# Kernel tuning notes

Measured on AMD Instinct MI355X. Metric: run time of the kernel, lower is better.

Reference implementation:

```python
import jax, jax.numpy as jnp
import numpy as np

LORA_ALPHA = 16.0

def setup_inputs() -> dict:
    key = jax.random.key(0)
    kx, kw, ka, kb, kbias = jax.random.split(key, 5)
    B_, S, D_in, D_out, R = 2, 4096, 4096, 4096, 16
    x = jax.random.normal(kx, (B_, S, D_in), dtype=jnp.float32)
    W = jax.random.normal(kw, (D_out, D_in), dtype=jnp.float32) * 0.02
    A = jax.random.normal(ka, (R, D_in), dtype=jnp.float32) * 0.02
    Bm = jax.random.normal(kb, (D_out, R), dtype=jnp.float32) * 0.02
    bias = jax.random.normal(kbias, (D_out,), dtype=jnp.float32) * 0.02
    return {"x": x, "W": W, "A": A, "B": Bm, "bias": bias}

def reference(x, W, A, B, bias):
    # y = x @ W.T + bias + (alpha/rank) * (x @ A.T) @ B.T   (dropout p=0)
    rank = A.shape[0]
    lora_scale = LORA_ALPHA / rank
    y = jnp.einsum('bsd,nd->bsn', x, W) + bias
    h = jnp.einsum('bsd,rd->bsr', x, A)          # [B,S,r] low-rank down-proj
    y = y + lora_scale * jnp.einsum('bsr,nr->bsn', h, B)
    return y
```

## Files before the change

### kernel.cpp

```cpp
#include <hip/hip_runtime.h>
#include <hip/hip_bf16.h>

typedef short bf16x8 __attribute__((ext_vector_type(8)));
typedef float f32x4 __attribute__((ext_vector_type(4)));
typedef unsigned short ushort8v __attribute__((ext_vector_type(8)));

#define SBAR() asm volatile("s_barrier" ::: "memory")
#define LGKM0() do { asm volatile("s_waitcnt lgkmcnt(0)" ::: "memory"); \
    __builtin_amdgcn_sched_barrier(0); } while (0)

__device__ __forceinline__ unsigned short f2bf(float f) {
  unsigned u = __builtin_bit_cast(unsigned, f);
  u += 0x7fffu + ((u >> 16) & 1u);
  return (unsigned short)(u >> 16);
}

__device__ __forceinline__ void gload_lds16(const unsigned short* g, unsigned short* l) {
  __builtin_amdgcn_global_load_lds((const __attribute__((address_space(1))) void*)g,
                                   (__attribute__((address_space(3))) void*)l, 16, 0, 0);
}

__global__ __launch_bounds__(256) void prep_kernel(const float* __restrict__ x,
                                                   const float* __restrict__ W,
                                                   const float* __restrict__ A,
                                                   const float* __restrict__ Bm,
                                                   unsigned short* __restrict__ xb,
                                                   unsigned short* __restrict__ wb,
                                                   float scale, int K, int R, int n8, int t8) {
  int i = blockIdx.x * 256 + threadIdx.x;
  if (i < n8) {
    const float4* p = (const float4*)x + (size_t)i * 2;
    float4 a = p[0], b = p[1];
    ushort8v v;
    v[0] = f2bf(a.x); v[1] = f2bf(a.y); v[2] = f2bf(a.z); v[3] = f2bf(a.w);
    v[4] = f2bf(b.x); v[5] = f2bf(b.y); v[6] = f2bf(b.z); v[7] = f2bf(b.w);
    *((ushort8v*)xb + i) = v;
    return;
  }
  int idx = i - n8;
  if (idx >= t8) return;
  int perRow = K >> 3;
  int n = idx / perRow;
  int d0 = (idx - n * perRow) << 3;
  const float4* wp = (const float4*)(W + (size_t)n * K + d0);
  float4 w0 = wp[0], w1 = wp[1];
  float acc[8] = {w0.x, w0.y, w0.z, w0.w, w1.x, w1.y, w1.z, w1.w};
#pragma unroll 4
  for (int r = 0; r < R; ++r) {
    float c = Bm[(size_t)n * R + r] * scale;
    const float4* ap = (const float4*)(A + (size_t)r * K + d0);
    float4 a0 = ap[0], a1 = ap[1];
    acc[0] += c * a0.x; acc[1] += c * a0.y; acc[2] += c * a0.z; acc[3] += c * a0.w;
    acc[4] += c * a1.x; acc[5] += c * a1.y; acc[6] += c * a1.z; acc[7] += c * a1.w;
  }
  ushort8v v;
#pragma unroll
  for (int j = 0; j < 8; ++j) v[j] = f2bf(acc[j]);
  *((ushort8v*)wb + idx) = v;
}

__global__ __launch_bounds__(512, 2) void gemm256_bt_bias(const unsigned short* __restrict__ Xb,
                                                          const unsigned short* __restrict__ Wb,
                                                          const float* __restrict__ bias,
                                                          float* __restrict__ C,
                                                          int M, int N, int K) {
  __shared__ __align__(16) unsigned short lds[4][16384];
  const int t = threadIdx.x;
  const int wave = t >> 6, lane = t & 63;
  const int fr = lane & 15, kc = lane >> 4;
  const int wr = wave >> 2, wc = wave & 3;

  const int NTn = N >> 8;
  const int nwg = gridDim.x;
  int bid = blockIdx.x;
  if ((nwg & 7) == 0) bid = (bid & 7) * (nwg >> 3) + (bid >> 3);
  const int tm = bid / NTn, tn = bid % NTn;
  const int m0 = tm << 8, n0 = tn << 8;

  const int srow = t >> 2;
  const int gch  = (t & 3) ^ ((t >> 3) & 3);
  const unsigned short* gA0 = Xb + (size_t)(m0 + srow) * K + gch * 8;
  const unsigned short* gA1 = gA0 + (size_t)128 * K;
  const unsigned short* gB0 = Wb + (size_t)(n0 + srow) * K + gch * 8;
  const unsigned short* gB1 = gB0 + (size_t)128 * K;
  const int stA0 = wave * 512;
  const int stA1 = 4096 + wave * 512;
  const int stB0 = 8192 + wave * 512;
  const int stB1 = 12288 + wave * 512;

  int offA[8], offB[4];
#pragma unroll
  for (int m = 0; m < 8; ++m) {
    int row = wr * 128 + m * 16 + fr;
    offA[m] = row * 64 + (((kc ^ (row >> 1)) & 3) << 4);
  }
#pragma unroll
  for (int n = 0; n < 4; ++n) {
    int row = wc * 64 + n * 16 + fr;
    offB[n] = 16384 + row * 64 + (((kc ^ (row >> 1)) & 3) << 4);
  }

  f32x4 acc[8][4];
#pragma unroll
  for (int m = 0; m < 8; ++m)
#pragma unroll
    for (int n = 0; n < 4; ++n) acc[m][n] = (f32x4){0.f, 0.f, 0.f, 0.f};

  const int NT = K >> 5;

#define STAGE_A(tt) do {                                 \
    unsigned short* sb_ = &lds[(tt) & 3][0];             \
    const int ko_ = (tt) * 32;                           \
    gload_lds16(gA0 + ko_, sb_ + stA0);                  \
    gload_lds16(gA1 + ko_, sb_ + stA1);                  \
  } while (0)
#define STAGE_B(tt) do {                                 \
    unsigned short* sb_ = &lds[(tt) & 3][0];             \
    const int ko_ = (tt) * 32;                           \
    gload_lds16(gB0 + ko_, sb_ + stB0);                  \
    gload_lds16(gB1 + ko_, sb_ + stB1);                  \
  } while (0)

#define TILE(tt, DOSTAGE, VM) do {                                                \
    const char* p_ = (const char*)&lds[(tt) & 3][0];                              \
    bf16x8 av_[4], bv_[4];                                                        \
    _Pragma("unroll") for (int n = 0; n < 4; ++n)                                 \
      bv_[n] = *(const bf16x8*)(p_ + offB[n]);                                    \
    _Pragma("unroll") for (int m = 0; m < 4; ++m)                                 \
      av_[m] = *(const bf16x8*)(p_ + offA[m]);                                    \
    if (DOSTAGE) { STAGE_A((tt) + 3); }                                           \
    SBAR();                                                                       \
    LGKM0();                                                                      \
    __builtin_amdgcn_s_setprio(1);                                                \
    _Pragma("unroll") for (int m = 0; m < 4; ++m)                                 \
      _Pragma("unroll") for (int n = 0; n < 4; ++n)                               \
        acc[m][n] = __builtin_amdgcn_mfma_f32_16x16x32_bf16(av_[m], bv_[n], acc[m][n], 0, 0, 0); \
    __builtin_amdgcn_s_setprio(0);                                                \
    SBAR();                                                                       \
    _Pragma("unroll") for (int m = 0; m < 4; ++m)                                 \
      av_[m] = *(const bf16x8*)(p_ + offA[4 + m]);                                \
    if (DOSTAGE) { STAGE_B((tt) + 3); }                                           \
    asm volatile("s_waitcnt vmcnt(" VM ")" ::: "memory");                         \
    SBAR();                                                                       \
    LGKM0();                                                                      \
    __builtin_amdgcn_s_setprio(1);                                                \
    _Pragma("unroll") for (int m = 0; m < 4; ++m)                                 \
      _Pragma("unroll") for (int n = 0; n < 4; ++n)                               \
        acc[4 + m][n] = __builtin_amdgcn_mfma_f32_16x16x32_bf16(av_[m], bv_[n], acc[4 + m][n], 0, 0, 0); \
    __builtin_amdgcn_s_setprio(0);                                                \
    SBAR();                                                                       \
  } while (0)

  STAGE_A(0); STAGE_B(0); STAGE_A(1); STAGE_B(1); STAGE_A(2); STAGE_B(2);
  asm volatile("s_waitcnt vmcnt(8)" ::: "memory");
  SBAR();

  for (int tt = 0; tt < NT - 3; ++tt) TILE(tt, 1, "8");
  TILE(NT - 3, 0, "4");
  TILE(NT - 2, 0, "0");
  TILE(NT - 1, 0, "0");

  const int crow = (lane >> 4) * 4;
  const int ccol = lane & 15;
#pragma unroll
  for (int n = 0; n < 4; ++n) {
    int col = n0 + wc * 64 + n * 16 + ccol;
    float bv = bias[col];
#pragma unroll
    for (int m = 0; m < 8; ++m) {
      int row = m0 + wr * 128 + m * 16 + crow;
      float* cp = C + (size_t)row * N + col;
#pragma unroll
      for (int r = 0; r < 4; ++r) cp[(size_t)r * N] = acc[m][n][r] + bv;
    }
  }
#undef STAGE_A
#undef STAGE_B
#undef TILE
}

__global__ __launch_bounds__(256) void gemm_bt_bias(const unsigned short* __restrict__ Xb,
                                                    const unsigned short* __restrict__ Wb,
                                                    const float* __restrict__ bias,
                                                    float* __restrict__ C,
                                                    int M, int N, int K) {
  __shared__ unsigned short sA[128 * 32];
  __shared__ unsigned short sB[128 * 32];
  const int t = threadIdx.x;
  const int wave = t >> 6, lane = t & 63;
  const int NT = N >> 7;
  const int nwg = gridDim.x;
  int bid = blockIdx.x;
  if ((nwg & 7) == 0) bid = (bid & 7) * (nwg >> 3) + (bid >> 3);
  const int tm = bid / NT, tn = bid % NT;
  const int m0 = tm << 7, n0 = tn << 7;
  const int wr = wave >> 1, wc = wave & 1;

  f32x4 acc[4][4];
#pragma unroll
  for (int m = 0; m < 4; ++m)
#pragma unroll
    for (int n = 0; n < 4; ++n) acc[m][n] = (f32x4){0.f, 0.f, 0.f, 0.f};

  const unsigned short* gA0 = Xb + (size_t)(m0 + (t >> 2)) * K + (t & 3) * 8;
  const unsigned short* gA1 = Xb + (size_t)(m0 + 64 + (t >> 2)) * K + (t & 3) * 8;
  const unsigned short* gB0 = Wb + (size_t)(n0 + (t >> 2)) * K + (t & 3) * 8;
  const unsigned short* gB1 = Wb + (size_t)(n0 + 64 + (t >> 2)) * K + (t & 3) * 8;
  unsigned short* lA0 = sA + (size_t)(wave * 64) * 8;
  unsigned short* lA1 = sA + (size_t)(256 + wave * 64) * 8;
  unsigned short* lB0 = sB + (size_t)(wave * 64) * 8;
  unsigned short* lB1 = sB + (size_t)(256 + wave * 64) * 8;

  const int rrow = lane & 15;
  const int rk = (lane >> 4) * 8;

  for (int k0 = 0; k0 < K; k0 += 32) {
    gload_lds16(gA0 + k0, lA0);
    gload_lds16(gA1 + k0, lA1);
    gload_lds16(gB0 + k0, lB0);
    gload_lds16(gB1 + k0, lB1);
    __syncthreads();
    bf16x8 af[4], bfr[4];
#pragma unroll
    for (int m = 0; m < 4; ++m)
      af[m] = *(const bf16x8*)&sA[(size_t)(wr * 64 + m * 16 + rrow) * 32 + rk];
#pragma unroll
    for (int n = 0; n < 4; ++n)
      bfr[n] = *(const bf16x8*)&sB[(size_t)(wc * 64 + n * 16 + rrow) * 32 + rk];
#pragma unroll
    for (int m = 0; m < 4; ++m)
#pragma unroll
      for (int n = 0; n < 4; ++n)
        acc[m][n] = __builtin_amdgcn_mfma_f32_16x16x32_bf16(af[m], bfr[n], acc[m][n], 0, 0, 0);
    __syncthreads();
  }
  const int crow0 = (lane >> 4) * 4;
  const int ccol = lane & 15;
#pragma unroll
  for (int n = 0; n < 4; ++n) {
    int col = n0 + wc * 64 + n * 16 + ccol;
    float bv = bias[col];
#pragma unroll
    for (int m = 0; m < 4; ++m) {
      int row = m0 + wr * 64 + m * 16 + crow0;
      float* cp = C + (size_t)row * N + col;
#pragma unroll
      for (int r = 0; r < 4; ++r) cp[(size_t)r * N] = acc[m][n][r] + bv;
    }
  }
}

__global__ __launch_bounds__(64) void lora_h_kernel(const float* __restrict__ x,
                                                    const float* __restrict__ A,
                                                    float* __restrict__ h,
                                                    float scale, int K, int R) {
  int m = blockIdx.x, lane = threadIdx.x;
  float acc[16];
#pragma unroll
  for (int r = 0; r < 16; ++r) acc[r] = 0.f;
  for (int d = lane; d < K; d += 64) {
    float xv = x[(size_t)m * K + d];
    for (int r = 0; r < R; ++r) acc[r] += xv * A[(size_t)r * K + d];
  }
  for (int off = 32; off; off >>= 1)
    for (int r = 0; r < R; ++r) acc[r] += __shfl_down(acc[r], off);
  if (lane == 0)
    for (int r = 0; r < R; ++r) h[(size_t)m * R + r] = acc[r] * scale;
}

__global__ __launch_bounds__(256) void fgemm_fallback(const float* __restrict__ X,
                                                      const float* __restrict__ W,
                                                      const float* __restrict__ Bm,
                                                      const float* __restrict__ bias,
                                                      const float* __restrict__ h,
                                                      float* __restrict__ C,
                                                      int M, int N, int K, int R) {
  __shared__ float sX[64][20];
  __shared__ float sW[64][20];
  int nt = N >> 6;
  int bx = blockIdx.x % nt, by = blockIdx.x / nt;
  int m0 = by << 6, n0 = bx << 6;
  int t = threadIdx.x;
  int tx = t & 15, ty = t >> 4;
  float acc[4][4] = {};
  int lr = t >> 2, lc = (t & 3) << 2;
  for (int k0 = 0; k0 < K; k0 += 16) {
    *(float4*)&sX[lr][lc] = *(const float4*)&X[(size_t)(m0 + lr) * K + k0 + lc];
    *(float4*)&sW[lr][lc] = *(const float4*)&W[(size_t)(n0 + lr) * K + k0 + lc];
    __syncthreads();
#pragma unroll
    for (int kk = 0; kk < 16; ++kk) {
      float a[4], b[4];
#pragma unroll
      for (int i = 0; i < 4; ++i) a[i] = sX[ty * 4 + i][kk];
#pragma unroll
      for (int j = 0; j < 4; ++j) b[j] = sW[tx * 4 + j][kk];
#pragma unroll
      for (int i = 0; i < 4; ++i)
#pragma unroll
        for (int j = 0; j < 4; ++j) acc[i][j] += a[i] * b[j];
    }
    __syncthreads();
  }
#pragma unroll
  for (int i = 0; i < 4; ++i) {
    int row = m0 + ty * 4 + i;
#pragma unroll
    for (int j = 0; j < 4; ++j) {
      int col = n0 + tx * 4 + j;
      float lo = 0.f;
      for (int r = 0; r < R; ++r) lo += h[(size_t)row * R + r] * Bm[(size_t)col * R + r];
      C[(size_t)row * N + col] = acc[i][j] + bias[col] + lo;
    }
  }
}

extern "C" void kernel_launch(void* const* d_in, const int* in_sizes, int n_in,
                              void* d_out, int out_size, void* d_ws, size_t ws_size,
                              hipStream_t stream) {
  const float* x    = (const float*)d_in[0];
  const float* W    = (const float*)d_in[1];
  const float* A    = (const float*)d_in[2];
  const float* Bm   = (const float*)d_in[3];
  const float* bias = (const float*)d_in[4];
  float* out = (float*)d_out;

  const int N = in_sizes[4];
  const int R = in_sizes[3] / N;
  const int K = in_sizes[2] / R;
  const int M = in_sizes[0] / K;
  const float scale = 16.0f / (float)R;

  const size_t xbytes = (size_t)M * K * 2;
  const size_t wbytes = (size_t)N * K * 2;
  const bool ws_ok = (ws_size >= xbytes + wbytes);
  const bool fast256 = ws_ok && (M % 256 == 0) && (N % 256 == 0) && (K % 32 == 0) && (K >= 128);
  const bool fast128 = ws_ok && (M % 128 == 0) && (N % 128 == 0) && (K % 32 == 0);

  if (fast256 || fast128) {
    unsigned short* xb = (unsigned short*)d_ws;
    unsigned short* wb = (unsigned short*)((char*)d_ws + xbytes);
    int n8 = M * K / 8;
    int t8 = N * K / 8;
    int total = n8 + t8;
    prep_kernel<<<dim3((total + 255) / 256), dim3(256), 0, stream>>>(x, W, A, Bm, xb, wb,
                                                                     scale, K, R, n8, t8);
    if (fast256) {
      int grid = (M / 256) * (N / 256);
      gemm256_bt_bias<<<dim3(grid), dim3(512), 0, stream>>>(xb, wb, bias, out, M, N, K);
    } else {
      int grid = (M / 128) * (N / 128);
      gemm_bt_bias<<<dim3(grid), dim3(256), 0, stream>>>(xb, wb, bias, out, M, N, K);
    }
  } else {
    float* h = (float*)d_ws;
    lora_h_kernel<<<dim3(M), dim3(64), 0, stream>>>(x, A, h, scale, K, R);
    int grid = (M / 64) * (N / 64);
    fgemm_fallback<<<dim3(grid), dim3(256), 0, stream>>>(x, W, Bm, bias, h, out, M, N, K, R);
  }
}
```

Baseline: 346.1 us.

## Software-pipeline LDS fragment reads across K tiles with double-buffered registers

Restructures the 256x256 GEMM main loop so the B fragments and first half of the A fragments for the next K tile are read from LDS during the current tile's second MFMA phase. Two register sets alternate across an unrolled-by-two loop, and full lgkmcnt(0) waits become partial waits. The aim is to hide LDS read latency behind MFMA work. It raises register pressure and requires K to be a multiple of 64.

```diff
diff --git a/kernel.cpp b/kernel.cpp
--- a/kernel.cpp
+++ b/kernel.cpp
@@ -6,8 +6,6 @@
 typedef unsigned short ushort8v __attribute__((ext_vector_type(8)));
 
 #define SBAR() asm volatile("s_barrier" ::: "memory")
-#define LGKM0() do { asm volatile("s_waitcnt lgkmcnt(0)" ::: "memory"); \
-    __builtin_amdgcn_sched_barrier(0); } while (0)
 
 __device__ __forceinline__ unsigned short f2bf(float f) {
   unsigned u = __builtin_bit_cast(unsigned, f);
@@ -108,6 +106,8 @@
 
   const int NT = K >> 5;
 
+  bf16x8 bv0[4], avA0[4], bv1[4], avA1[4], avB[4];
+
 #define STAGE_A(tt) do {                                 \
     unsigned short* sb_ = &lds[(tt) & 3][0];             \
     const int ko_ = (tt) * 32;                           \
@@ -120,33 +120,41 @@
     gload_lds16(gB0 + ko_, sb_ + stB0);                  \
     gload_lds16(gB1 + ko_, sb_ + stB1);                  \
   } while (0)
-
-#define TILE(tt, DOSTAGE, VM) do {                                                \
+#define READ_BV_AVA(tt, BV, AVA) do {                                             \
     const char* p_ = (const char*)&lds[(tt) & 3][0];                              \
-    bf16x8 av_[4], bv_[4];                                                        \
     _Pragma("unroll") for (int n = 0; n < 4; ++n)                                 \
-      bv_[n] = *(const bf16x8*)(p_ + offB[n]);                                    \
+      BV[n] = *(const bf16x8*)(p_ + offB[n]);                                     \
     _Pragma("unroll") for (int m = 0; m < 4; ++m)                                 \
-      av_[m] = *(const bf16x8*)(p_ + offA[m]);                                    \
+      AVA[m] = *(const bf16x8*)(p_ + offA[m]);                                    \
+  } while (0)
+
+#define TILE(tt, BVc, AVAc, BVn, AVAn, DOSTAGE, VM, DONEXT) do {                  \
+    { const char* p_ = (const char*)&lds[(tt) & 3][0];                            \
+      _Pragma("unroll") for (int m = 0; m < 4; ++m)                               \
+        avB[m] = *(const bf16x8*)(p_ + offA[4 + m]); }                            \
     if (DOSTAGE) { STAGE_A((tt) + 3); }                                           \
     SBAR();                                                                       \
-    LGKM0();                                                                      \
+    asm volatile("s_waitcnt lgkmcnt(4)" ::: "memory");       \
+    __builtin_amdgcn_sched_barrier(0);                                            \
     __builtin_amdgcn_s_setprio(1);                                                \
     _Pragma("unroll") for (int m = 0; m < 4; ++m)                                 \
       _Pragma("unroll") for (int n = 0; n < 4; ++n)                               \
-        acc[m][n] = __builtin_amdgcn_mfma_f32_16x16x32_bf16(av_[m], bv_[n], acc[m][n], 0, 0, 0); \
+        acc[m][n] = __builtin_amdgcn_mfma_f32_16x16x32_bf16(AVAc[m], BVc[n], acc[m][n], 0, 0, 0); \
     __builtin_amdgcn_s_setprio(0);                                                \
     SBAR();                                                                       \
-    _Pragma("unroll") for (int m = 0; m < 4; ++m)                                 \
-      av_[m] = *(const bf16x8*)(p_ + offA[4 + m]);                                \
     if (DOSTAGE) { STAGE_B((tt) + 3); }                                           \
-    asm volatile("s_waitcnt vmcnt(" VM ")" ::: "memory");                         \
-    SBAR();                                                                       \
-    LGKM0();                                                                      \
+    asm volatile("s_waitcnt vmcnt(" VM ")" ::: "memory");   \
+    SBAR();                                            \
+    if (DONEXT) { READ_BV_AVA((tt) + 1, BVn, AVAn);                               \
+      asm volatile("s_waitcnt lgkmcnt(8)" ::: "memory");          \
+    } else {                                                                      \
+      asm volatile("s_waitcnt lgkmcnt(0)" ::: "memory");                          \
+    }                                                                             \
+    __builtin_amdgcn_sched_barrier(0);                                            \
     __builtin_amdgcn_s_setprio(1);                                                \
     _Pragma("unroll") for (int m = 0; m < 4; ++m)                                 \
       _Pragma("unroll") for (int n = 0; n < 4; ++n)                               \
-        acc[4 + m][n] = __builtin_amdgcn_mfma_f32_16x16x32_bf16(av_[m], bv_[n], acc[4 + m][n], 0, 0, 0); \
+        acc[4 + m][n] = __builtin_amdgcn_mfma_f32_16x16x32_bf16(avB[m], BVc[n], acc[4 + m][n], 0, 0, 0); \
     __builtin_amdgcn_s_setprio(0);                                                \
     SBAR();                                                                       \
   } while (0)
@@ -154,11 +162,17 @@
   STAGE_A(0); STAGE_B(0); STAGE_A(1); STAGE_B(1); STAGE_A(2); STAGE_B(2);
   asm volatile("s_waitcnt vmcnt(8)" ::: "memory");
   SBAR();
-
-  for (int tt = 0; tt < NT - 3; ++tt) TILE(tt, 1, "8");
-  TILE(NT - 3, 0, "4");
-  TILE(NT - 2, 0, "0");
-  TILE(NT - 1, 0, "0");
+  READ_BV_AVA(0, bv0, avA0);
+
+  int tt = 0;
+  for (; tt + 5 < NT; tt += 2) {
+    TILE(tt,     bv0, avA0, bv1, avA1, 1, "8", 1);
+    TILE(tt + 1, bv1, avA1, bv0, avA0, 1, "8", 1);
+  }
+  TILE(NT - 4, bv0, avA0, bv1, avA1, 1, "8", 1);
+  TILE(NT - 3, bv1, avA1, bv0, avA0, 0, "4", 1);
+  TILE(NT - 2, bv0, avA0, bv1, avA1, 0, "0", 1);
+  TILE(NT - 1, bv1, avA1, bv0, avA0, 0, "0", 0);
 
   const int crow = (lane >> 4) * 4;
   const int ccol = lane & 15;
@@ -176,6 +190,7 @@
   }
 #undef STAGE_A
 #undef STAGE_B
+#undef READ_BV_AVA
 #undef TILE
 }
 
@@ -334,7 +349,7 @@
   const size_t xbytes = (size_t)M * K * 2;
   const size_t wbytes = (size_t)N * K * 2;
   const bool ws_ok = (ws_size >= xbytes + wbytes);
-  const bool fast256 = ws_ok && (M % 256 == 0) && (N % 256 == 0) && (K % 32 == 0) && (K >= 128);
+  const bool fast256 = ws_ok && (M % 256 == 0) && (N % 256 == 0) && (K % 64 == 0) && (K >= 128);
   const bool fast128 = ws_ok && (M % 128 == 0) && (N % 128 == 0) && (K % 32 == 0);
 
   if (fast256 || fast128) {
```

Result: no change. 340.9 us (-1.5%).

## Restructure 256x256 GEMM main loop to K=64 steps with double-buffered quadrant MFMA schedule

Applied to the files above, without the earlier changes.

The 256x256 bf16 GEMM now advances K by 64 per step instead of 32. It uses two 64 KB LDS buffers with an 8-way XOR swizzle in place of four 32 KB stages. Each K step is split into four quadrant MFMA phases, with the A and B global-to-LDS stages interleaved between them and B prefetched two steps ahead. The aim is fewer barriers per unit of work and better overlap of loads with MFMAs, at the cost of 128 KB of LDS per block, which may limit occupancy to one block per CU, and a stricter K%64 requirement.

```diff
diff --git a/kernel.cpp b/kernel.cpp
--- a/kernel.cpp
+++ b/kernel.cpp
@@ -64,7 +64,7 @@
                                                           const float* __restrict__ bias,
                                                           float* __restrict__ C,
                                                           int M, int N, int K) {
-  __shared__ __align__(16) unsigned short lds[4][16384];
+  __shared__ __align__(16) char lds[131072];
   const int t = threadIdx.x;
   const int wave = t >> 6, lane = t & 63;
   const int fr = lane & 15, kc = lane >> 4;
@@ -77,28 +77,19 @@
   const int tm = bid / NTn, tn = bid % NTn;
   const int m0 = tm << 8, n0 = tn << 8;
 
-  const int srow = t >> 2;
-  const int gch  = (t & 3) ^ ((t >> 3) & 3);
-  const unsigned short* gA0 = Xb + (size_t)(m0 + srow) * K + gch * 8;
-  const unsigned short* gA1 = gA0 + (size_t)128 * K;
-  const unsigned short* gB0 = Wb + (size_t)(n0 + srow) * K + gch * 8;
-  const unsigned short* gB1 = gB0 + (size_t)128 * K;
-  const int stA0 = wave * 512;
-  const int stA1 = 4096 + wave * 512;
-  const int stB0 = 8192 + wave * 512;
-  const int stB1 = 12288 + wave * 512;
-
-  int offA[8], offB[4];
-#pragma unroll
-  for (int m = 0; m < 8; ++m) {
-    int row = wr * 128 + m * 16 + fr;
-    offA[m] = row * 64 + (((kc ^ (row >> 1)) & 3) << 4);
-  }
-#pragma unroll
-  for (int n = 0; n < 4; ++n) {
-    int row = wc * 64 + n * 16 + fr;
-    offB[n] = 16384 + row * 64 + (((kc ^ (row >> 1)) & 3) << 4);
-  }
+  const int grow = t >> 3;
+  const int gch8 = ((t & 7) ^ ((t >> 3) & 7)) << 3;
+  const unsigned short* gA0 = Xb + (size_t)(m0 + grow) * K + gch8;
+  const unsigned short* gB0 = Wb + (size_t)(n0 + grow) * K + gch8;
+  char* stg = (char*)lds + wave * 1024;
+
+  const int sw  = (lane & 7) << 4;
+  const int cb0 = (kc << 4) ^ sw;
+  const int cb1 = ((4 + kc) << 4) ^ sw;
+  const int oA0 = (wr * 128 + fr) * 128 + cb0;
+  const int oA1 = (wr * 128 + fr) * 128 + cb1;
+  const int oB0 = 32768 + (wc * 64 + fr) * 128 + cb0;
+  const int oB1 = 32768 + (wc * 64 + fr) * 128 + cb1;
 
   f32x4 acc[8][4];
 #pragma unroll
@@ -106,59 +97,63 @@
 #pragma unroll
     for (int n = 0; n < 4; ++n) acc[m][n] = (f32x4){0.f, 0.f, 0.f, 0.f};
 
-  const int NT = K >> 5;
-
-#define STAGE_A(tt) do {                                 \
-    unsigned short* sb_ = &lds[(tt) & 3][0];             \
-    const int ko_ = (tt) * 32;                           \
-    gload_lds16(gA0 + ko_, sb_ + stA0);                  \
-    gload_lds16(gA1 + ko_, sb_ + stA1);                  \
+  bf16x8 aQa[8], aQb[8], bQ0[4], bQ1[4];
+  const int NT = K >> 6;
+
+#define STG_A(s, step) gload_lds16(gA0 + (size_t)(s) * 64 * K + (size_t)(step) * 64, \
+    (unsigned short*)(stg + (((step) & 1) << 16) + (s) * 8192))
+#define STG_B(s, step) gload_lds16(gB0 + (size_t)(s) * 64 * K + (size_t)(step) * 64, \
+    (unsigned short*)(stg + (((step) & 1) << 16) + 32768 + (s) * 8192))
+
+#define RD_A(dst, qmo, p_) do { \
+    dst[0]=*(const bf16x8*)((p_)+oA0+(qmo));      dst[1]=*(const bf16x8*)((p_)+oA1+(qmo)); \
+    dst[2]=*(const bf16x8*)((p_)+oA0+(qmo)+2048); dst[3]=*(const bf16x8*)((p_)+oA1+(qmo)+2048); \
+    dst[4]=*(const bf16x8*)((p_)+oA0+(qmo)+4096); dst[5]=*(const bf16x8*)((p_)+oA1+(qmo)+4096); \
+    dst[6]=*(const bf16x8*)((p_)+oA0+(qmo)+6144); dst[7]=*(const bf16x8*)((p_)+oA1+(qmo)+6144); } while (0)
+#define RD_B(dst, qno, p_) do { \
+    dst[0]=*(const bf16x8*)((p_)+oB0+(qno));      dst[1]=*(const bf16x8*)((p_)+oB1+(qno)); \
+    dst[2]=*(const bf16x8*)((p_)+oB0+(qno)+2048); dst[3]=*(const bf16x8*)((p_)+oB1+(qno)+2048); } while (0)
+
+#define MM(qm, qn, AR, BR) do { \
+    __builtin_amdgcn_s_setprio(1); \
+    _Pragma("unroll") for (int ks = 0; ks < 2; ++ks) \
+    _Pragma("unroll") for (int m = 0; m < 4; ++m) \
+    _Pragma("unroll") for (int n = 0; n < 2; ++n) \
+      acc[(qm)*4+m][(qn)*2+n] = __builtin_amdgcn_mfma_f32_16x16x32_bf16( \
+          AR[m*2+ks], BR[n*2+ks], acc[(qm)*4+m][(qn)*2+n], 0, 0, 0); \
+    __builtin_amdgcn_s_setprio(0); } while (0)
+
+#define KSTEP(c, STA, STB, VM) do { \
+    const char* p_ = (const char*)lds + (((c) & 1) << 16); \
+     \
+    RD_A(aQa, 0, p_); RD_B(bQ0, 0, p_); \
+    if (STA) { STG_A(0, (c) + 1); STG_A(1, (c) + 1); } \
+    asm volatile("s_waitcnt lgkmcnt(8)" ::: "memory"); \
+    SBAR(); LGKM0(); MM(0, 0, aQa, bQ0); SBAR(); \
+     \
+    RD_B(bQ1, 4096, p_); \
+    if (STA) { STG_A(2, (c) + 1); STG_A(3, (c) + 1); } \
+    SBAR(); LGKM0(); MM(0, 1, aQa, bQ1); SBAR(); \
+     \
+    RD_A(aQb, 8192, p_); \
+    if (STB) { STG_B(0, (c) + 2); STG_B(1, (c) + 2); } \
+    SBAR(); LGKM0(); MM(1, 0, aQb, bQ0); SBAR(); \
+     \
+    if (STB) { STG_B(2, (c) + 2); STG_B(3, (c) + 2); } \
+    asm volatile("s_waitcnt vmcnt(" VM ")" ::: "memory"); \
+    SBAR(); MM(1, 1, aQb, bQ1); SBAR(); \
   } while (0)
-#define STAGE_B(tt) do {                                 \
-    unsigned short* sb_ = &lds[(tt) & 3][0];             \
-    const int ko_ = (tt) * 32;                           \
-    gload_lds16(gB0 + ko_, sb_ + stB0);                  \
-    gload_lds16(gB1 + ko_, sb_ + stB1);                  \
-  } while (0)
-
-#define TILE(tt, DOSTAGE, VM) do {                                                \
-    const char* p_ = (const char*)&lds[(tt) & 3][0];                              \
-    bf16x8 av_[4], bv_[4];                                                        \
-    _Pragma("unroll") for (int n = 0; n < 4; ++n)                                 \
-      bv_[n] = *(const bf16x8*)(p_ + offB[n]);                                    \
-    _Pragma("unroll") for (int m = 0; m < 4; ++m)                                 \
-      av_[m] = *(const bf16x8*)(p_ + offA[m]);                                    \
-    if (DOSTAGE) { STAGE_A((tt) + 3); }                                           \
-    SBAR();                                                                       \
-    LGKM0();                                                                      \
-    __builtin_amdgcn_s_setprio(1);                                                \
-    _Pragma("unroll") for (int m = 0; m < 4; ++m)                                 \
-      _Pragma("unroll") for (int n = 0; n < 4; ++n)                               \
-        acc[m][n] = __builtin_amdgcn_mfma_f32_16x16x32_bf16(av_[m], bv_[n], acc[m][n], 0, 0, 0); \
-    __builtin_amdgcn_s_setprio(0);                                                \
-    SBAR();                                                                       \
-    _Pragma("unroll") for (int m = 0; m < 4; ++m)                                 \
-      av_[m] = *(const bf16x8*)(p_ + offA[4 + m]);                                \
-    if (DOSTAGE) { STAGE_B((tt) + 3); }                                           \
-    asm volatile("s_waitcnt vmcnt(" VM ")" ::: "memory");                         \
-    SBAR();                                                                       \
-    LGKM0();                                                                      \
-    __builtin_amdgcn_s_setprio(1);                                                \
-    _Pragma("unroll") for (int m = 0; m < 4; ++m)                                 \
-      _Pragma("unroll") for (int n = 0; n < 4; ++n)                               \
-        acc[4 + m][n] = __builtin_amdgcn_mfma_f32_16x16x32_bf16(av_[m], bv_[n], acc[4 + m][n], 0, 0, 0); \
-    __builtin_amdgcn_s_setprio(0);                                                \
-    SBAR();                                                                       \
-  } while (0)
-
-  STAGE_A(0); STAGE_B(0); STAGE_A(1); STAGE_B(1); STAGE_A(2); STAGE_B(2);
-  asm volatile("s_waitcnt vmcnt(8)" ::: "memory");
+
+  STG_A(0, 0); STG_A(1, 0); STG_A(2, 0); STG_A(3, 0);
+  STG_B(0, 0); STG_B(1, 0); STG_B(2, 0); STG_B(3, 0);
+  STG_B(0, 1); STG_B(1, 1); STG_B(2, 1); STG_B(3, 1);
+  asm volatile("s_waitcnt vmcnt(4)" ::: "memory");
   SBAR();
 
-  for (int tt = 0; tt < NT - 3; ++tt) TILE(tt, 1, "8");
-  TILE(NT - 3, 0, "4");
-  TILE(NT - 2, 0, "0");
-  TILE(NT - 1, 0, "0");
+  int c = 0;
+  for (; c < NT - 2; ++c) KSTEP(c, 1, 1, "4");
+  KSTEP(NT - 2, 1, 0, "0");
+  KSTEP(NT - 1, 0, 0, "0");
 
   const int crow = (lane >> 4) * 4;
   const int ccol = lane & 15;
@@ -174,9 +169,12 @@
       for (int r = 0; r < 4; ++r) cp[(size_t)r * N] = acc[m][n][r] + bv;
     }
   }
-#undef STAGE_A
-#undef STAGE_B
-#undef TILE
+#undef STG_A
+#undef STG_B
+#undef RD_A
+#undef RD_B
+#undef MM
+#undef KSTEP
 }
 
 __global__ __launch_bounds__(256) void gemm_bt_bias(const unsigned short* __restrict__ Xb,
@@ -334,7 +332,7 @@
   const size_t xbytes = (size_t)M * K * 2;
   const size_t wbytes = (size_t)N * K * 2;
   const bool ws_ok = (ws_size >= xbytes + wbytes);
-  const bool fast256 = ws_ok && (M % 256 == 0) && (N % 256 == 0) && (K % 32 == 0) && (K >= 128);
+  const bool fast256 = ws_ok && (M % 256 == 0) && (N % 256 == 0) && (K % 64 == 0) && (K >= 128);
   const bool fast128 = ws_ok && (M % 128 == 0) && (N % 128 == 0) && (K % 32 == 0);
 
   if (fast256 || fast128) {
```

After: 330.7 us. -4.4%, faster.
